# Kernel tuning notes

Measured on AMD Instinct MI355X. Metric: run time of the kernel, lower is better.

Reference implementation:

```python
import jax, jax.numpy as jnp
import numpy as np


def _log_g(x):
    # numerically stable log of g(x) = where(x>=0, x+0.5, sigmoid(x))
    return jnp.where(x >= 0, jnp.log(jax.nn.relu(x) + 0.5), -jax.nn.softplus(-x))


def setup_inputs() -> dict:
    key = jax.random.key(0)
    k1, k2, k3, k4 = jax.random.split(key, 4)
    B, T, D = 4, 4096, 1024
    Di = 2 * D  # dim_inner = int(dim * expansion_factor), expansion_factor = 2.0
    x = jax.random.normal(k1, (B, T, D), dtype=jnp.float32)
    prev_hidden = jax.random.uniform(k2, (B, Di), dtype=jnp.float32)  # positive carry state
    # torch Linear(dim, 2*dim_inner, bias=False): stored here pre-transposed as [D, 2*Di]
    W_hg = jax.random.normal(k3, (D, 2 * Di), dtype=jnp.float32) * (1.0 / np.sqrt(D))
    # out_proj Linear(dim_inner, dim, bias=False): stored pre-transposed as [Di, D]
    W_out = jax.random.normal(k4, (Di, D), dtype=jnp.float32) * (1.0 / np.sqrt(Di))
    return {"x": x, "prev_hidden": prev_hidden, "W_hg": W_hg, "W_out": W_out}


def reference(x, prev_hidden, W_hg, W_out):
    # x: [B, T, D]; prev_hidden: [B, Di] (positive)
    T = x.shape[1]
    hg = jnp.einsum('btd,de->bte', x, W_hg)          # [B, T, 2*Di]
    hidden, gate = jnp.split(hg, 2, axis=-1)          # each [B, T, Di]

    # Heinsen log-space affine scan: h_t = (1 - z_t) * h_{t-1} + z_t * g(hidden_t)
    log_coeffs = -jax.nn.softplus(gate)               # log(1 - sigmoid(gate))
    log_values = -jax.nn.softplus(-gate) + _log_g(hidden)  # log(sigmoid(gate)) + log g(hidden)

    # prepend carry state
    prev_log = jnp.clip(jnp.log(jnp.clip(prev_hidden, 1e-8, None)), -30.0, None)[:, None]  # [B,1,Di]
    log_values = jnp.concatenate([prev_log, log_values], axis=1)      # [B, T+1, Di]
    log_coeffs = jnp.pad(log_coeffs, ((0, 0), (1, 0), (0, 0)))        # [B, T+1, Di]

    a_star = jnp.cumsum(log_coeffs, axis=1)
    h = jnp.exp(a_star + jax.lax.cumlogsumexp(log_values - a_star, axis=1))  # [B, T+1, Di]
    h = h[:, -T:]                                     # drop carry slot

    next_hidden = h[:, -1]                            # [B, Di]
    out = jnp.einsum('bte,ed->btd', h, W_out)         # [B, T, D]
    return (out, next_hidden)
```

## Files before the change

### kernel.cpp

```cpp
#include <hip/hip_runtime.h>
#include <cstdio>

#define T_LEN 4096
#define B_SZ  4
#define D_IN  1024
#define DI    2048
#define MM    16384
#define NC2   128
#define CHL2  32

typedef __attribute__((ext_vector_type(8))) __bf16 bf16x8;
typedef __attribute__((ext_vector_type(4))) float  f32x4;
typedef __attribute__((ext_vector_type(8))) unsigned short u16x8;

__device__ __forceinline__ unsigned short f2bf(float f){
  unsigned u = __builtin_bit_cast(unsigned, f);
  u += 0x7fffu + ((u >> 16) & 1u);
  return (unsigned short)(u >> 16);
}
__device__ __forceinline__ float bf2f_lo(unsigned u){
  return __builtin_bit_cast(float, u << 16);
}
__device__ __forceinline__ float bf2f_hi(unsigned u){
  return __builtin_bit_cast(float, u & 0xffff0000u);
}
__device__ __forceinline__ float bf2f_s(unsigned short s){
  return __builtin_bit_cast(float, (unsigned)s << 16);
}

__device__ __forceinline__ void async16(void* lds, const void* g){
  __builtin_amdgcn_global_load_lds((const __attribute__((address_space(1))) void*)g,
                                   (__attribute__((address_space(3))) void*)lds, 16, 0, 0);
}

template<int PERM>
__device__ __forceinline__ void transpose_body(const float* __restrict__ src,
                                               unsigned short* __restrict__ dst,
                                               int n0, int k0, int SK, int SN,
                                               float (*tile)[65], int tid){
  #pragma unroll
  for(int it=0; it<16; it++){
    int idx = it*256 + tid;
    int kk = idx>>6, nn = idx&63;
    int n = n0+nn;
    int col = PERM ? (((n>>5)<<4) + (n&15) + ((n&16)?2048:0)) : n;
    tile[kk][nn] = src[(size_t)(k0+kk)*SN + col];
  }
  __syncthreads();
  #pragma unroll
  for(int it=0; it<16; it++){
    int idx = it*256 + tid;
    int nn = idx>>6, kk = idx&63;
    dst[(size_t)(n0+nn)*SK + k0+kk] = f2bf(tile[kk][nn]);
  }
}

__global__ __launch_bounds__(256) void k_prep(const float* __restrict__ x,
                                              unsigned short* __restrict__ xb,
                                              const float* __restrict__ Whg,
                                              unsigned short* __restrict__ wt,
                                              const float* __restrict__ Wout,
                                              unsigned short* __restrict__ wo){
  __shared__ float tile[64][65];
  int bid = blockIdx.x, tid = threadIdx.x;
  if(bid < 8192){
    size_t t = (size_t)bid*256 + tid;
    const float4* xi = (const float4*)x;
    float4 a = xi[2*t], b = xi[2*t+1];
    u16x8 o;
    o[0]=f2bf(a.x); o[1]=f2bf(a.y); o[2]=f2bf(a.z); o[3]=f2bf(a.w);
    o[4]=f2bf(b.x); o[5]=f2bf(b.y); o[6]=f2bf(b.z); o[7]=f2bf(b.w);
    ((u16x8*)xb)[t] = o;
  } else if(bid < 9216){
    int j = bid - 8192;
    transpose_body<1>(Whg, wt, (j&63)*64, (j>>6)*64, 1024, 4096, tile, tid);
  } else {
    int j = bid - 9216;
    transpose_body<0>(Wout, wo, (j&15)*64, (j>>4)*64, 2048, 1024, tile, tid);
  }
}

template<int EPI>
__global__ __launch_bounds__(256, 2)
void k_gemm(const unsigned short* __restrict__ A, const unsigned short* __restrict__ Bt,
            float* __restrict__ C0, unsigned* __restrict__ U0,
            unsigned* __restrict__ U1, unsigned short* __restrict__ Ap,
            unsigned short* __restrict__ Vp, int M, int N, int K){
  __shared__ unsigned short lsA[(EPI==0) ? 19456 : 8192];
  __shared__ unsigned short lsB[128*64];
  int tid  = threadIdx.x;
  int lane = tid & 63, wave = tid >> 6;
  int wm = wave >> 1, wn = wave & 1;
  int cl = lane & 15, quad = lane >> 4;

  int m0, n0;
  if(EPI==1){
    m0 = blockIdx.y * 128; n0 = blockIdx.x * 128;
  } else {
    int gx = gridDim.x;
    int nwg = gx * gridDim.y;
    int orig = blockIdx.y * gx + blockIdx.x;
    int swz = (orig & 7) * (nwg >> 3) + (orig >> 3);
    int lg = 31 - __clz(gx);
    int bx = swz & (gx - 1), by = swz >> lg;
    m0 = by * 128; n0 = bx * 128;
  }

  f32x4 acc[4][4];
  #pragma unroll
  for(int i=0;i<4;i++)
    #pragma unroll
    for(int j=0;j<4;j++) acc[i][j] = (f32x4){0.f,0.f,0.f,0.f};

  int g = (tid&7) ^ ((tid>>3)&7);
  const unsigned short* gA = A  + (size_t)(m0 + (tid>>3))*K + g*8;
  const unsigned short* gB = Bt + (size_t)(n0 + (tid>>3))*K + g*8;
  unsigned short* dA = lsA + tid*8;
  unsigned short* dB = lsB + tid*8;

  for(int k0=0; k0<K; k0+=64){
    #pragma unroll
    for(int it=0; it<4; it++){
      async16(dA + it*2048, gA + (size_t)(it*32)*K + k0);
      async16(dB + it*2048, gB + (size_t)(it*32)*K + k0);
    }
    __syncthreads();
    #pragma unroll
    for(int kh=0; kh<2; kh++){
      bf16x8 fa[4], fb[4];
      int sl = ((kh<<2)|quad);
      #pragma unroll
      for(int t2=0;t2<4;t2++){
        int ra = wm*64 + t2*16 + cl;
        int rb = wn*64 + t2*16 + cl;
        fa[t2] = *(const bf16x8*)&lsA[ra*64 + (sl^(cl&7))*8];
        fb[t2] = *(const bf16x8*)&lsB[rb*64 + (sl^(cl&7))*8];
      }
      #pragma unroll
      for(int i=0;i<4;i++)
        #pragma unroll
        for(int j=0;j<4;j++)
          acc[i][j] = __builtin_amdgcn_mfma_f32_16x16x32_bf16(fa[i], fb[j], acc[i][j], 0, 0, 0);
    }
    __syncthreads();
  }

  if(EPI==0){
    #pragma unroll
    for(int i=0;i<4;i++)
      #pragma unroll
      for(int j=0;j<4;j++){
        int n = n0 + wn*64 + j*16 + cl;
        #pragma unroll
        for(int r=0;r<4;r++){
          int m = m0 + wm*64 + i*16 + quad*4 + r;
          C0[(size_t)m*N + n] = acc[i][j][r];
        }
      }
  } else {
    float* lA_f = (float*)lsA;
    float* lV_f = (float*)lsB;
    int ibase = ((n0 + wn*64) >> 1) + cl;
    int odd = cl & 1;
    #pragma unroll
    for(int i=0;i<4;i++)
      #pragma unroll
      for(int p=0;p<2;p++){
        f32x4 hh = acc[i][2*p], gg = acc[i][2*p+1];
        int ii = ibase + p*16;
        float pa = 1.f, pv = 0.f;
        #pragma unroll
        for(int r=0;r<4;r++){
          int m = m0 + wm*64 + i*16 + quad*4 + r;
          float gate = gg[r], hid = hh[r];
          float e  = __expf(gate);
          float cc = 1.f/(1.f + e);
          float z  = (gate > 80.f) ? 1.f : e*cc;
          float gv = (hid >= 0.f) ? (hid + 0.5f) : (1.f/(1.f + __expf(-hid)));
          float vv = z*gv;
          float ccp = __shfl_xor(cc, 1, 64);
          float vvp = __shfl_xor(vv, 1, 64);
          unsigned wlo = odd ? (unsigned)f2bf(vvp) : (unsigned)f2bf(cc);
          unsigned whi = odd ? (unsigned)f2bf(vv)  : (unsigned)f2bf(ccp);
          unsigned* dst = odd ? U1 : U0;
          dst[((size_t)m*DI + (ii & ~1)) >> 1] = wlo | (whi << 16);
          pa *= cc;
          pv = fmaf(cc, pv, vv);
        }
        int seg = wm*16 + i*4 + quad;
        int chl = wn*32 + p*16 + cl;
        lA_f[seg*64 + chl] = pa;
        lV_f[seg*64 + chl] = pv;
      }
    __syncthreads();
    {
      int ch = tid & 63, q = tid >> 6;
      float Ac = 1.f, Vc = 0.f;
      #pragma unroll
      for(int s=0; s<8; s++){
        int idx = (q*8 + s)*64 + ch;
        float a = lA_f[idx], v = lV_f[idx];
        Ac *= a;
        Vc = fmaf(a, Vc, v);
      }
      int b = m0 >> 12;
      int ch32 = ((m0 & 4095) >> 5) + q;
      size_t o = (size_t)(b*NC2 + ch32)*DI + (n0 >> 1) + ch;
      Ap[o] = f2bf(Ac); Vp[o] = f2bf(Vc);
    }
  }
}

__global__ __launch_bounds__(256) void k_scanB(const float* __restrict__ prev,
                                               unsigned short* __restrict__ Ap,
                                               const unsigned short* __restrict__ Vp){
  int t = blockIdx.x*256 + threadIdx.x;
  int i = t & (DI-1); int b = t >> 11;
  float h = fmaxf(prev[t], 1e-8f);
  for(int ch=0; ch<NC2; ch++){
    size_t o = (size_t)(b*NC2 + ch)*DI + i;
    float a = bf2f_s(Ap[o]), vv = bf2f_s(Vp[o]);
    Ap[o] = f2bf(h);
    h = fmaf(a, h, vv);
  }
}

__global__ __launch_bounds__(256) void k_scanC(const uint4* __restrict__ cp,
                                               uint4* __restrict__ vp,
                                               const uint4* __restrict__ hinp,
                                               float* __restrict__ nh){
  int t = blockIdx.x*256 + threadIdx.x;
  int i8 = t & (DI/8 - 1);
  int ch = (t >> 8) & (NC2-1);
  int b  = t >> 15;
  size_t base = ((size_t)(b*T_LEN + ch*CHL2))*(DI/8) + i8;
  uint4 hp = hinp[(size_t)(b*NC2 + ch)*(DI/8) + i8];
  float h0 = bf2f_lo(hp.x), h1 = bf2f_hi(hp.x);
  float h2 = bf2f_lo(hp.y), h3 = bf2f_hi(hp.y);
  float h4 = bf2f_lo(hp.z), h5 = bf2f_hi(hp.z);
  float h6 = bf2f_lo(hp.w), h7 = bf2f_hi(hp.w);
  #pragma unroll 4
  for(int s=0; s<CHL2; s++){
    uint4 cu = cp[base], vu = vp[base];
    h0 = fmaf(bf2f_lo(cu.x), h0, bf2f_lo(vu.x));
    h1 = fmaf(bf2f_hi(cu.x), h1, bf2f_hi(vu.x));
    h2 = fmaf(bf2f_lo(cu.y), h2, bf2f_lo(vu.y));
    h3 = fmaf(bf2f_hi(cu.y), h3, bf2f_hi(vu.y));
    h4 = fmaf(bf2f_lo(cu.z), h4, bf2f_lo(vu.z));
    h5 = fmaf(bf2f_hi(cu.z), h5, bf2f_hi(vu.z));
    h6 = fmaf(bf2f_lo(cu.w), h6, bf2f_lo(vu.w));
    h7 = fmaf(bf2f_hi(cu.w), h7, bf2f_hi(vu.w));
    uint4 o;
    o.x = (unsigned)f2bf(h0) | ((unsigned)f2bf(h1) << 16);
    o.y = (unsigned)f2bf(h2) | ((unsigned)f2bf(h3) << 16);
    o.z = (unsigned)f2bf(h4) | ((unsigned)f2bf(h5) << 16);
    o.w = (unsigned)f2bf(h6) | ((unsigned)f2bf(h7) << 16);
    vp[base] = o;
    base += DI/8;
  }
  if(ch == NC2-1){
    float* d = nh + (size_t)b*DI + 8*i8;
    d[0]=h0; d[1]=h1; d[2]=h2; d[3]=h3; d[4]=h4; d[5]=h5; d[6]=h6; d[7]=h7;
  }
}

extern "C" void kernel_launch(void* const* d_in, const int* in_sizes, int n_in,
                              void* d_out, int out_size, void* d_ws, size_t ws_size,
                              hipStream_t stream){
  const float* x    = (const float*)d_in[0];
  const float* prev = (const float*)d_in[1];
  const float* Whg  = (const float*)d_in[2];
  const float* Wout = (const float*)d_in[3];
  float* out = (float*)d_out;
  float* nh  = out + (size_t)MM*D_IN;

  const size_t NEED = 117440512;
  if(ws_size < NEED){
    fprintf(stderr, "kernel_launch: ws_size=%zu < needed %zu — aborting launch\n",
            ws_size, NEED);
    return;
  }
  char* ws = (char*)d_ws;
  unsigned short* xb = (unsigned short*)(ws);
  unsigned short* wt = (unsigned short*)(ws + 33554432);
  unsigned short* wo = (unsigned short*)(ws + 41943040);
  unsigned short* v  = (unsigned short*)(ws + 46137344);
  unsigned short* Ap = (unsigned short*)(ws + 113246208);
  unsigned short* Vp = (unsigned short*)(ws + 115343360);
  unsigned* c = (unsigned*)d_out;

  k_prep<<<9728, 256, 0, stream>>>(x, xb, Whg, wt, Wout, wo);

  k_gemm<1><<<dim3(32,128), 256, 0, stream>>>(xb, wt, nullptr, c, (unsigned*)v,
                                              Ap, Vp, MM, 2*DI, D_IN);

  k_scanB<<<32,   256, 0, stream>>>(prev, Ap, Vp);
  k_scanC<<<512,  256, 0, stream>>>((const uint4*)c, (uint4*)v,
                                    (const uint4*)Ap, nh);

  k_gemm<0><<<dim3(8,128), 256, 0, stream>>>(v, wo, out, nullptr, nullptr,
                                             nullptr, nullptr, MM, D_IN, DI);
}
```

Baseline: 406.5 us.

## Parallelize chunk-carry scan across warps with two-level hierarchical scan

The middle scan kernel previously had one thread per channel walking all 128 chunk carries serially, launched on only 32 blocks. It now splits the 128 chunks into 8 groups of 16 handled by separate warps. Each warp composes its group's affine transforms, one warp scans the 8 group summaries through shared memory, and every warp then writes its prefix states. The launch grows to 256 blocks. This cuts the serial dependency chain and raises occupancy, at the cost of extra register arrays, two barriers, and 32-wide channel accesses that coalesce less well.

```diff
diff --git a/kernel.cpp b/kernel.cpp
--- a/kernel.cpp
+++ b/kernel.cpp
@@ -214,14 +214,38 @@
 __global__ __launch_bounds__(256) void k_scanB(const float* __restrict__ prev,
                                                unsigned short* __restrict__ Ap,
                                                const unsigned short* __restrict__ Vp){
-  int t = blockIdx.x*256 + threadIdx.x;
-  int i = t & (DI-1); int b = t >> 11;
-  float h = fmaxf(prev[t], 1e-8f);
-  for(int ch=0; ch<NC2; ch++){
-    size_t o = (size_t)(b*NC2 + ch)*DI + i;
-    float a = bf2f_s(Ap[o]), vv = bf2f_s(Vp[o]);
-    Ap[o] = f2bf(h);
-    h = fmaf(a, h, vv);
+  int tid = threadIdx.x;
+  int cl = tid & 31;
+  int g  = tid >> 5;
+  int chan = blockIdx.x*32 + cl;
+  int i = chan & (DI-1); int b = chan >> 11;
+  size_t o0 = (size_t)(b*NC2 + g*16)*DI + i;
+  float a[16], v[16];
+  #pragma unroll
+  for(int j=0;j<16;j++){
+    a[j] = bf2f_s(Ap[o0 + (size_t)j*DI]);
+    v[j] = bf2f_s(Vp[o0 + (size_t)j*DI]);
+  }
+  float A = 1.f, V = 0.f;
+  #pragma unroll
+  for(int j=0;j<16;j++){ A *= a[j]; V = fmaf(a[j], V, v[j]); }
+  __shared__ float sA[8][32], sV[8][32], sH[8][32];
+  sA[g][cl] = A; sV[g][cl] = V;
+  __syncthreads();
+  if(g == 0){
+    float h = fmaxf(prev[chan], 1e-8f);
+    #pragma unroll
+    for(int j=0;j<8;j++){
+      sH[j][cl] = h;
+      h = fmaf(sA[j][cl], h, sV[j][cl]);
+    }
+  }
+  __syncthreads();
+  float h = sH[g][cl];
+  #pragma unroll
+  for(int j=0;j<16;j++){
+    Ap[o0 + (size_t)j*DI] = f2bf(h);
+    h = fmaf(a[j], h, v[j]);
   }
 }
 
@@ -294,7 +318,7 @@
   k_gemm<1><<<dim3(32,128), 256, 0, stream>>>(xb, wt, nullptr, c, (unsigned*)v,
                                               Ap, Vp, MM, 2*DI, D_IN);
 
-  k_scanB<<<32,   256, 0, stream>>>(prev, Ap, Vp);
+  k_scanB<<<256,  256, 0, stream>>>(prev, Ap, Vp);
   k_scanC<<<512,  256, 0, stream>>>((const uint4*)c, (uint4*)v,
                                     (const uint4*)Ap, nh);
 
```

Result: faster. 391.5 us (-3.7%).
